# Kernel tuning notes

Measured on AMD Instinct MI355X. Metric: run time of the kernel, lower is better.

The kernel has to match this reference:

```python
import jax, jax.numpy as jnp
import numpy as np
from jax import lax

T, B, D_IN, H = 512, 128, 512, 512


def setup_inputs() -> dict:
    key = jax.random.key(0)
    k1, k2, k3, k4 = jax.random.split(key, 4)
    ins = jax.random.normal(k1, (T, B, D_IN), dtype=jnp.float32)
    resets = jax.random.bernoulli(k2, 0.05, (T, B))  # episode-boundary reset mask
    carry = jnp.zeros((B, H), dtype=jnp.float32)
    # fused GRU weights: gate order (r, z, n); input denses have no bias in flax GRUCell
    Wi = jax.random.normal(k3, (D_IN, 3 * H), dtype=jnp.float32) * (1.0 / np.sqrt(D_IN))
    Wh = jax.random.normal(k4, (H, 3 * H), dtype=jnp.float32) * (1.0 / np.sqrt(H))
    bh = jnp.zeros((3 * H,), dtype=jnp.float32)
    return {"carry": carry, "ins": ins, "resets": resets, "Wi": Wi, "Wh": Wh, "bh": bh}


def reference(carry, ins, resets, Wi, Wh, bh):
    """ScannedRNN forward: scan a flax GRUCell over time with per-step reset masking.

    Returns (final_carry [B,H], ys [T,B,H]).
    """

    def step(h, xr):
        x, r_mask = xr                       # x: [B,D_in], r_mask: [B]
        h = jnp.where(r_mask[:, None], jnp.zeros_like(h), h)
        gi = x @ Wi                          # [B,3H]  (no input bias in flax GRUCell)
        gh = h @ Wh + bh                     # [B,3H]
        ir, iz, inn = jnp.split(gi, 3, axis=-1)
        hr, hz, hn = jnp.split(gh, 3, axis=-1)
        r = jax.nn.sigmoid(ir + hr)
        z = jax.nn.sigmoid(iz + hz)
        n = jnp.tanh(inn + r * hn)
        new_h = (1.0 - z) * n + z * h
        return new_h, new_h                  # GRUCell returns (new_carry, new_carry)

    final_carry, ys = lax.scan(step, carry, (ins, resets))
    return final_carry, ys
```

## Files before the change

### kernel.cpp

```cpp
#include <hip/hip_runtime.h>

#define T_STEPS 512
#define BATCH   128
#define DIN     512
#define HDIM    512
#define THREEH  1536
#define THREADS 256
#define LDK     520
#define LDG     49
#define NGROUP  4
#define NSLICE  32
#define BC      32
#define HC      16
#define NC      48
#define CNT_STRIDE 16
#define SPIN_MAX (1 << 16)
#define EX_DWORDS (NSLICE * BATCH * HC / 2)
#define NG4 8
#define RW4 16
#define NS4 32
#define EXSLOT 131072
#define FLAGS_OFF  0
#define GBAR_OFF   1088
#define DEC_OFF    1280
#define VD_OFF     2048
#define HS_OFF     3072
#define EX_OFF     4096
#define GI_OFF     (1u<<20)
#define GI_BYTES   201326592ULL

typedef _Float16 half8 __attribute__((ext_vector_type(8)));
typedef _Float16 half4v __attribute__((ext_vector_type(4)));
typedef float    f32x4 __attribute__((ext_vector_type(4)));
typedef unsigned int uint4v __attribute__((ext_vector_type(4)));

__global__ void sniff_kernel(const unsigned int* __restrict__ w,
                             unsigned int* __restrict__ dec) {
  unsigned int local = 0;
  for (int i = threadIdx.x; i < (T_STEPS * BATCH) / 4; i += THREADS) {
    if (w[i] > 1u) local = 1u;
  }
  if (local) atomicOr(dec, 1u);
}

__device__ __forceinline__ void run_gemm(const _Float16* __restrict__ sAa,
                                         const _Float16* __restrict__ sW,
                                         float* __restrict__ sAcc,
                                         int wid, int lane) {
  const int fr = lane & 15;
  const int kb = (lane >> 4) * 8;
  for (int tile = wid; tile < 6; tile += 4) {
    int mi = tile / 3, ni = tile - mi * 3;
    const _Float16* ap = sAa + (mi * 16 + fr) * LDK + kb;
    const _Float16* bp = sW  + (ni * 16 + fr) * LDK + kb;
    f32x4 acc = {0.f, 0.f, 0.f, 0.f};
#pragma unroll
    for (int kk = 0; kk < DIN / 32; ++kk)
      acc = __builtin_amdgcn_mfma_f32_16x16x32_f16(
          *(const half8*)(ap + kk * 32),
          *(const half8*)(bp + kk * 32), acc, 0, 0, 0);
    int crow = mi * 16 + (lane >> 4) * 4;
    int ccol = ni * 16 + fr;
#pragma unroll
    for (int j = 0; j < 4; ++j) sAcc[(crow + j) * LDG + ccol] = acc[j];
  }
}

__global__ __launch_bounds__(THREADS, 1)
void gru_kernel_v1(const float* __restrict__ carry,
                   const float* __restrict__ ins,
                   const void*  __restrict__ resets_raw,
                   const float* __restrict__ Wi,
                   const float* __restrict__ Wh,
                   const float* __restrict__ bh,
                   float* __restrict__ out,
                   unsigned int* __restrict__ cnt,
                   unsigned int* __restrict__ ex0,
                   unsigned int* __restrict__ ex1,
                   const unsigned int* __restrict__ dec)
{
  __shared__ alignas(16) _Float16 sWi[NC * LDK];
  __shared__ alignas(16) _Float16 sWh[NC * LDK];
  __shared__ alignas(16) _Float16 sA [BC * LDK];
  __shared__ float sGi[BC * LDG];
  __shared__ float sGh[BC * LDG];
  __shared__ float sBh[NC];
  __shared__ int   sRst[BC];

  const int tid  = threadIdx.x;
  const int bid  = blockIdx.x;
  const int g    = bid & (NGROUP - 1);
  const int p    = bid >> 2;
  const int row0 = g * BC;
  const int col0 = p * HC;

  float* carryOut = out;
  float* ys = out + BATCH * HDIM;

  const unsigned int isBool = *dec;
  const unsigned char* r8  = (const unsigned char*)resets_raw;
  const int*           r32 = (const int*)resets_raw;

  unsigned int* ex[2] = { ex0, ex1 };
  unsigned int* myCnt = cnt + g * CNT_STRIDE;

  for (int idx = tid; idx < DIN * NC; idx += THREADS) {
    int k  = idx / NC;
    int ci = idx - k * NC;
    int gcol = (ci >> 4) * HDIM + col0 + (ci & 15);
    sWi[ci * LDK + k] = (_Float16)Wi[k * THREEH + gcol];
    sWh[ci * LDK + k] = (_Float16)Wh[k * THREEH + gcol];
  }
  if (tid < NC) {
    int gcol = (tid >> 4) * HDIM + col0 + (tid & 15);
    sBh[tid] = bh[gcol];
  }

  float hreg[2];
  {
    int idx = tid * 2;
    int b0 = idx >> 4, c0 = idx & 15;
    hreg[0] = carry[(size_t)(row0 + b0) * HDIM + col0 + c0];
    hreg[1] = carry[(size_t)(row0 + b0) * HDIM + col0 + c0 + 1];
  }

  const int wid  = tid >> 6;
  const int lane = tid & 63;

  auto stageRst = [&](int t) {
    if (tid < BC) {
      int off = t * BATCH + row0 + tid;
      sRst[tid] = isBool ? (int)r8[off] : r32[off];
    }
  };
  auto stageX = [&](int t) {
    const float4* src = (const float4*)(ins + (size_t)(t * BATCH + row0) * DIN);
    for (int i = tid; i < BC * (DIN / 4); i += THREADS) {
      int r = i >> 7, c4 = i & 127;
      float4 v = src[(size_t)r * 128 + c4];
      half4v hv = {(_Float16)v.x, (_Float16)v.y, (_Float16)v.z, (_Float16)v.w};
      *(half4v*)&sA[r * LDK + c4 * 4] = hv;
    }
  };

  stageRst(0);
  stageX(0);
  __syncthreads();
  run_gemm(sA, sWi, sGi, wid, lane);
  __syncthreads();
  {
    const float4* src = (const float4*)(carry + (size_t)row0 * HDIM);
    for (int i = tid; i < BC * (HDIM / 4); i += THREADS) {
      int r = i >> 7, c4 = i & 127;
      float4 v = src[(size_t)r * 128 + c4];
      float m = sRst[r] ? 0.f : 1.f;
      half4v hv = {(_Float16)(v.x*m), (_Float16)(v.y*m),
                   (_Float16)(v.z*m), (_Float16)(v.w*m)};
      *(half4v*)&sA[r * LDK + c4 * 4] = hv;
    }
  }
  __syncthreads();

  for (int t = 0; t < T_STEPS; ++t) {
    if (t > 0) {
      {
        const unsigned int target = 32u * (unsigned)t;
        unsigned int fv;
        for (int it = 0; it < SPIN_MAX; ++it) {
          asm volatile("global_load_dword %0, %1, off sc0 sc1\n\t"
                       "s_waitcnt vmcnt(0)"
                       : "=v"(fv) : "v"(myCnt) : "memory");
          if (fv >= target) break;
          __builtin_amdgcn_s_sleep(1);
        }
      }
      {
        const unsigned int* exsrc = ex[(t - 1) & 1];
        uint4v vv[8];
#pragma unroll
        for (int j = 0; j < 8; ++j) {
          int i = tid + THREADS * j;
          int p_ = i >> 6, b_ = (i >> 1) & 31, hw = (i & 1) << 2;
          const unsigned int* sp = exsrc + p_ * 1024 + (row0 + b_) * 8 + hw;
          asm volatile("global_load_dwordx4 %0, %1, off sc0 sc1"
                       : "=&v"(vv[j]) : "v"(sp) : "memory");
        }
        asm volatile("s_waitcnt vmcnt(0)" ::: "memory");
        __builtin_amdgcn_sched_barrier(0);
#pragma unroll
        for (int j = 0; j < 8; ++j) {
          int i = tid + THREADS * j;
          int p_ = i >> 6, b_ = (i >> 1) & 31, hw = (i & 1) << 3;
          half8 hv = *reinterpret_cast<half8*>(&vv[j]);
          half8 z = {(_Float16)0, (_Float16)0, (_Float16)0, (_Float16)0,
                     (_Float16)0, (_Float16)0, (_Float16)0, (_Float16)0};
          hv = sRst[b_] ? z : hv;
          *(half8*)&sA[b_ * LDK + p_ * 16 + hw] = hv;
        }
      }
      __syncthreads();
    }

    run_gemm(sA, sWh, sGh, wid, lane);
    __syncthreads();

    {
#pragma unroll
      for (int e = 0; e < 2; ++e) {
        int idx = tid * 2 + e;
        int b = idx >> 4, cj = idx & 15;
        float gir = sGi[b * LDG + cj];
        float giz = sGi[b * LDG + 16 + cj];
        float gin = sGi[b * LDG + 32 + cj];
        float ghr = sGh[b * LDG + cj]      + sBh[cj];
        float ghz = sGh[b * LDG + 16 + cj] + sBh[16 + cj];
        float ghn = sGh[b * LDG + 32 + cj] + sBh[32 + cj];
        float r = 1.f / (1.f + __expf(-(gir + ghr)));
        float z = 1.f / (1.f + __expf(-(giz + ghz)));
        float n = tanhf(gin + r * ghn);
        float hp = sRst[b] ? 0.f : hreg[e];
        hreg[e] = (1.f - z) * n + z * hp;
      }
      union { _Float16 h[2]; unsigned int u; } pk;
      pk.h[0] = (_Float16)hreg[0];
      pk.h[1] = (_Float16)hreg[1];
      unsigned int* dst = ex[t & 1] + p * 1024 + (row0 + (tid >> 3)) * 8 + (tid & 7);
      asm volatile("global_store_dword %0, %1, off sc0 sc1"
                   :: "v"(dst), "v"(pk.u) : "memory");
      int b0 = (tid * 2) >> 4, c0 = (tid * 2) & 15;
      float2 yv = make_float2(hreg[0], hreg[1]);
      *(float2*)&ys[((size_t)t * BATCH + row0 + b0) * HDIM + col0 + c0] = yv;
      if (t == T_STEPS - 1)
        *(float2*)&carryOut[(size_t)(row0 + b0) * HDIM + col0 + c0] = yv;
    }
    asm volatile("s_waitcnt vmcnt(0)" ::: "memory");
    __syncthreads();
    if (tid == 0) atomicAdd(myCnt, 1u);

    if (t < T_STEPS - 1) {
      stageRst(t + 1);
      stageX(t + 1);
      __syncthreads();
      run_gemm(sA, sWi, sGi, wid, lane);
      __syncthreads();
    }
  }
}

__global__ __launch_bounds__(256, 1)
void gi_prepass2(const float* __restrict__ ins,
                 const float* __restrict__ Wi,
                 _Float16* __restrict__ gis)
{
  __shared__ alignas(16) _Float16 sWiT[48 * LDK];
  __shared__ alignas(16) _Float16 sX[32 * LDK];

  const int tid = threadIdx.x;
  const int bid = blockIdx.x;
  const int n   = bid >> 3;
  const int mg  = bid & 7;
  const int wid = tid >> 6;
  const int lane = tid & 63;
  const int fr = lane & 15;
  const int kb = (lane >> 4) * 8;

  for (int idx = tid; idx < 48 * DIN; idx += 256) {
    int ci = idx % 48, k = idx / 48;
    int gcol = (ci >> 4) * HDIM + n * 16 + (ci & 15);
    sWiT[ci * LDK + k] = (_Float16)Wi[(size_t)k * THREEH + gcol];
  }

  float4 va[16];
  auto LOADS = [&](int ch) {
    const float4* src = (const float4*)(ins + (size_t)(mg * 8192 + ch * 32) * DIN);
#pragma unroll
    for (int j = 0; j < 16; ++j) va[j] = src[tid + 256 * j];
  };
  auto WRITE = [&]() {
#pragma unroll
    for (int j = 0; j < 16; ++j) {
      int i = tid + 256 * j;
      int r = i >> 7, c4 = i & 127;
      float4 v = va[j];
      half4v hv = {(_Float16)v.x, (_Float16)v.y, (_Float16)v.z, (_Float16)v.w};
      *(half4v*)&sX[r * LDK + c4 * 4] = hv;
    }
  };

  LOADS(0);
  for (int ch = 0; ch < 256; ++ch) {
    WRITE();
    __syncthreads();
    if (ch + 1 < 256) LOADS(ch + 1);

    const int m0 = mg * 8192 + ch * 32;
    const int tt = m0 >> 7;
    const int bb0 = m0 & 127;
    for (int tile = wid; tile < 6; tile += 4) {
      int mi = tile / 3, ni = tile - mi * 3;
      const _Float16* ap = sX   + (mi * 16 + fr) * LDK + kb;
      const _Float16* bp = sWiT + (ni * 16 + fr) * LDK + kb;
      f32x4 acc = {0.f, 0.f, 0.f, 0.f};
#pragma unroll
      for (int kk = 0; kk < DIN / 32; ++kk)
        acc = __builtin_amdgcn_mfma_f32_16x16x32_f16(
            *(const half8*)(ap + kk * 32),
            *(const half8*)(bp + kk * 32), acc, 0, 0, 0);
      int gr = mi * 16 + ((lane >> 4) << 2);
      int col = n * 16 + fr;
      size_t base = ((size_t)(tt * 3 + ni) * BATCH) * HDIM + col;
#pragma unroll
      for (int j = 0; j < 4; ++j)
        gis[base + (size_t)(bb0 + gr + j) * HDIM] = (_Float16)acc[j];
    }
    __syncthreads();
  }
}

__device__ __forceinline__ void gridbar(unsigned int* ctr, int tid) {
  __syncthreads();
  if (tid == 0) {
    atomicAdd(ctr, 1u);
    unsigned int v;
    for (int it = 0; it < SPIN_MAX; ++it) {
      asm volatile("global_load_dword %0, %1, off sc0 sc1\n\t"
                   "s_waitcnt vmcnt(0)" : "=v"(v) : "v"(ctr) : "memory");
      if (v >= 256u) break;
      __builtin_amdgcn_s_sleep(1);
    }
  }
  __syncthreads();
}

__global__ __launch_bounds__(256, 1)
void gru_kernel_v4(const float* __restrict__ carry,
                   const void*  __restrict__ resets_raw,
                   const float* __restrict__ Wh,
                   const float* __restrict__ bh,
                   float* __restrict__ out,
                   unsigned int* __restrict__ wsb,
                   const _Float16* __restrict__ gis,
                   const unsigned int* __restrict__ dec)
{
  __shared__ alignas(16) _Float16 sWh[NC * LDK];
  __shared__ alignas(16) _Float16 sA [RW4 * LDK];
  __shared__ float sGh[RW4 * LDG];
  __shared__ float sBh[NC];
  __shared__ int   sRst[RW4];
  __shared__ int   sFast;

  const int tid  = threadIdx.x;
  const int bid  = blockIdx.x;
  const int g    = bid & 7;
  const int p    = bid >> 3;
  const int row0 = g * RW4;
  const int col0 = p * HC;

  unsigned int* flags = wsb + (FLAGS_OFF / 4) ;
  unsigned int* gbars = wsb + (GBAR_OFF / 4);
  unsigned int* vd    = wsb + (VD_OFF / 4);
  unsigned int* hs    = wsb + (HS_OFF / 4);
  char*         exb   = (char*)wsb + EX_OFF;

  float* carryOut = out;
  float* ys = out + BATCH * HDIM;

  const unsigned int isBool = *dec;
  const unsigned char* r8  = (const unsigned char*)resets_raw;
  const int*           r32 = (const int*)resets_raw;

  bool ok1 = true, ok2 = true;
  {
    unsigned int PAT1 = 0xC0DE0000u | (unsigned)bid;
    unsigned int PAT2 = 0xFACE0000u | (unsigned)bid;
    if (tid == 0) {
      unsigned int* hp = hs + bid;
      asm volatile("global_store_dword %0, %1, off sc0\n\t"
                   "s_waitcnt vmcnt(0)" :: "v"(hp), "v"(PAT1) : "memory");
    }
    gridbar(gbars + 0 * 16, tid);
    if (tid < 32) {
      int peer = g + 8 * tid;
      unsigned int v;
      const unsigned int* hp = hs + peer;
      asm volatile("global_load_dword %0, %1, off sc0\n\t"
                   "s_waitcnt vmcnt(0)" : "=v"(v) : "v"(hp) : "memory");
      ok1 = (v == (0xC0DE0000u | (unsigned)peer));
    }
    gridbar(gbars + 1 * 16, tid);
    if (tid == 0) {
      unsigned int* hp = hs + bid;
      asm volatile("global_store_dword %0, %1, off sc0\n\t"
                   "s_waitcnt vmcnt(0)" :: "v"(hp), "v"(PAT2) : "memory");
    }
    gridbar(gbars + 2 * 16, tid);
    if (tid < 32) {
      int peer = g + 8 * tid;
      unsigned int v;
      const unsigned int* hp = hs + peer;
      asm volatile("global_load_dword %0, %1, off sc0\n\t"
                   "s_waitcnt vmcnt(0)" : "=v"(v) : "v"(hp) : "memory");
      ok2 = (v == (0xFACE0000u | (unsigned)peer));
    }
    bool myok = (tid < 32) ? (ok1 && ok2) : true;
    bool wgok = __all(myok);
    if (tid == 0) {
      unsigned int vv = wgok ? 1u : 0u;
      unsigned int* vp = vd + bid;
      asm volatile("global_store_dword %0, %1, off sc0 sc1\n\t"
                   "s_waitcnt vmcnt(0)" :: "v"(vp), "v"(vv) : "memory");
    }
    gridbar(gbars + 3 * 16, tid);
    bool fin = true;
    if (tid < 32) {
      int peer = g + 8 * tid;
      unsigned int v;
      const unsigned int* vp = vd + peer;
      asm volatile("global_load_dword %0, %1, off sc0 sc1\n\t"
                   "s_waitcnt vmcnt(0)" : "=v"(v) : "v"(vp) : "memory");
      fin = (v == 1u);
    }
    bool unan = __all((tid < 32) ? fin : true);
    if (tid == 0) sFast = unan ? 1 : 0;
    __syncthreads();
  }
  const int fast = sFast;

  if (tid == 0) {
    unsigned int* fp = flags + (g * 32 + p);
    unsigned int zz = 0u;
    if (fast) {
      asm volatile("global_store_dword %0, %1, off sc0\n\t"
                   "s_waitcnt vmcnt(0)" :: "v"(fp), "v"(zz) : "memory");
    } else {
      asm volatile("global_store_dword %0, %1, off sc0 sc1\n\t"
                   "s_waitcnt vmcnt(0)" :: "v"(fp), "v"(zz) : "memory");
    }
  }
  gridbar(gbars + 4 * 16, tid);

  for (int idx = tid; idx < DIN * NC; idx += THREADS) {
    int k  = idx / NC;
    int ci = idx - k * NC;
    int gcol = (ci >> 4) * HDIM + col0 + (ci & 15);
    sWh[ci * LDK + k] = (_Float16)Wh[k * THREEH + gcol];
  }
  if (tid < NC) {
    int gcol = (tid >> 4) * HDIM + col0 + (tid & 15);
    sBh[tid] = bh[gcol];
  }

  const int gb = tid >> 4;
  const int gc = tid & 15;
  float hreg = carry[(size_t)(row0 + gb) * HDIM + col0 + gc];

  const int wid  = tid >> 6;
  const int lane = tid & 63;
  const int fr   = lane & 15;
  const int kb   = (lane >> 4) * 8;

  if (tid < RW4) {
    int off = row0 + tid;
    sRst[tid] = isBool ? (int)r8[off] : r32[off];
  }
  __syncthreads();
  {
    const float4* src = (const float4*)(carry + (size_t)row0 * HDIM);
    for (int i = tid; i < RW4 * (HDIM / 4); i += THREADS) {
      int r = i >> 7, c4 = i & 127;
      float4 v = src[(size_t)r * 128 + c4];
      float m = sRst[r] ? 0.f : 1.f;
      half4v hv = {(_Float16)(v.x*m), (_Float16)(v.y*m),
                   (_Float16)(v.z*m), (_Float16)(v.w*m)};
      *(half4v*)&sA[r * LDK + c4 * 4] = hv;
    }
  }

  const unsigned short* gisu = (const unsigned short*)gis;

  for (int t = 0; t < T_STEPS; ++t) {
    unsigned short gu0, gu1, gu2;
    {
      size_t base = ((size_t)(t * 3) * BATCH + row0 + gb) * HDIM + col0 + gc;
      gu0 = gisu[base];
      gu1 = gisu[base + (size_t)BATCH * HDIM];
      gu2 = gisu[base + 2 * (size_t)BATCH * HDIM];
    }
    if (t > 0 && tid < RW4) {
      int off = t * BATCH + row0 + tid;
      sRst[tid] = isBool ? (int)r8[off] : r32[off];
    }
    if (t > 0) {
      bool done = false;
      const unsigned int* fp = flags + (g * 32 + (tid & 31));
      for (int it = 0; it < SPIN_MAX && !done; ++it) {
        unsigned int fv = 0xFFFFFFFFu;
        if (tid < 32) {
          if (fast) {
            asm volatile("global_load_dword %0, %1, off sc0\n\t"
                         "s_waitcnt vmcnt(0)" : "=v"(fv) : "v"(fp) : "memory");
          } else {
            asm volatile("global_load_dword %0, %1, off sc0 sc1\n\t"
                         "s_waitcnt vmcnt(0)" : "=v"(fv) : "v"(fp) : "memory");
          }
        }
        done = __all((tid < 32) ? (fv >= (unsigned)t) : true);
        if (!done) __builtin_amdgcn_s_sleep(1);
      }
    }
    __syncthreads();

    if (t > 0) {
      const char* src = exb + ((t - 1) & 1) * EXSLOT + g * 16384
                      + (tid >> 4) * 1024 + (tid & 15) * 64;
      uint4v v0, v1, v2, v3;
      if (fast) {
        asm volatile("global_load_dwordx4 %0, %4, off sc0\n\t"
                     "global_load_dwordx4 %1, %4, off offset:16 sc0\n\t"
                     "global_load_dwordx4 %2, %4, off offset:32 sc0\n\t"
                     "global_load_dwordx4 %3, %4, off offset:48 sc0\n\t"
                     "s_waitcnt vmcnt(0)"
                     : "=&v"(v0), "=&v"(v1), "=&v"(v2), "=&v"(v3)
                     : "v"(src) : "memory");
      } else {
        asm volatile("global_load_dwordx4 %0, %4, off sc0 sc1\n\t"
                     "global_load_dwordx4 %1, %4, off offset:16 sc0 sc1\n\t"
                     "global_load_dwordx4 %2, %4, off offset:32 sc0 sc1\n\t"
                     "global_load_dwordx4 %3, %4, off offset:48 sc0 sc1\n\t"
                     "s_waitcnt vmcnt(0)"
                     : "=&v"(v0), "=&v"(v1), "=&v"(v2), "=&v"(v3)
                     : "v"(src) : "memory");
      }
      __builtin_amdgcn_sched_barrier(0);
      int r = tid >> 4, c0 = (tid & 15) * 32;
      half8 h0 = *reinterpret_cast<half8*>(&v0);
      half8 h1 = *reinterpret_cast<half8*>(&v1);
      half8 h2 = *reinterpret_cast<half8*>(&v2);
      half8 h3 = *reinterpret_cast<half8*>(&v3);
      half8 z = {(_Float16)0, (_Float16)0, (_Float16)0, (_Float16)0,
                 (_Float16)0, (_Float16)0, (_Float16)0, (_Float16)0};
      if (sRst[r]) { h0 = z; h1 = z; h2 = z; h3 = z; }
      *(half8*)&sA[r * LDK + c0 +  0] = h0;
      *(half8*)&sA[r * LDK + c0 +  8] = h1;
      *(half8*)&sA[r * LDK + c0 + 16] = h2;
      *(half8*)&sA[r * LDK + c0 + 24] = h3;
      __syncthreads();
    }

    if (wid < 3) {
      const int ni = wid;
      const _Float16* ap = sA  + fr * LDK + kb;
      const _Float16* bp = sWh + (ni * 16 + fr) * LDK + kb;
      f32x4 a0 = {0.f, 0.f, 0.f, 0.f}, a1 = {0.f, 0.f, 0.f, 0.f};
#pragma unroll
      for (int kk = 0; kk < DIN / 32; kk += 2) {
        a0 = __builtin_amdgcn_mfma_f32_16x16x32_f16(
            *(const half8*)(ap + kk * 32), *(const half8*)(bp + kk * 32), a0, 0, 0, 0);
        a1 = __builtin_amdgcn_mfma_f32_16x16x32_f16(
            *(const half8*)(ap + (kk + 1) * 32), *(const half8*)(bp + (kk + 1) * 32), a1, 0, 0, 0);
      }
      a0 += a1;
      int crow = (lane >> 4) * 4;
      int ccol = ni * 16 + fr;
#pragma unroll
      for (int j = 0; j < 4; ++j) sGh[(crow + j) * LDG + ccol] = a0[j];
    }
    __syncthreads();

    {
      union { unsigned short u; _Float16 h; } c0_, c1_, c2_;
      c0_.u = gu0; c1_.u = gu1; c2_.u = gu2;
      float gir = (float)c0_.h;
      float giz = (float)c1_.h;
      float gin = (float)c2_.h;
      float ghr = sGh[gb * LDG + gc]      + sBh[gc];
      float ghz = sGh[gb * LDG + 16 + gc] + sBh[16 + gc];
      float ghn = sGh[gb * LDG + 32 + gc] + sBh[32 + gc];
      float r = 1.f / (1.f + __expf(-(gir + ghr)));
      float z = 1.f / (1.f + __expf(-(giz + ghz)));
      float n = tanhf(gin + r * ghn);
      float hp = sRst[gb] ? 0.f : hreg;
      hreg = (1.f - z) * n + z * hp;

      union { _Float16 h; unsigned short u; } pk;
      pk.h = (_Float16)hreg;
      unsigned int pv = (unsigned int)pk.u;
      unsigned short* dst = (unsigned short*)
        (exb + (t & 1) * EXSLOT + g * 16384 + gb * 1024 + (col0 + gc) * 2);
      if (fast) {
        asm volatile("global_store_short %0, %1, off sc0"
                     :: "v"(dst), "v"(pv) : "memory");
      } else {
        asm volatile("global_store_short %0, %1, off sc0 sc1"
                     :: "v"(dst), "v"(pv) : "memory");
      }
    }
    asm volatile("s_waitcnt vmcnt(0)" ::: "memory");
    __syncthreads();
    if (tid == 0) {
      unsigned int* fp = flags + (g * 32 + p);
      unsigned int val = (unsigned)(t + 1);
      if (fast) {
        asm volatile("global_store_dword %0, %1, off sc0"
                     :: "v"(fp), "v"(val) : "memory");
      } else {
        asm volatile("global_store_dword %0, %1, off sc0 sc1"
                     :: "v"(fp), "v"(val) : "memory");
      }
    }
    {
      ys[((size_t)t * BATCH + row0 + gb) * HDIM + col0 + gc] = hreg;
      if (t == T_STEPS - 1)
        carryOut[(size_t)(row0 + gb) * HDIM + col0 + gc] = hreg;
    }
  }

  __builtin_amdgcn_fence(__ATOMIC_RELEASE, "agent");
}

extern "C" void kernel_launch(void* const* d_in, const int* in_sizes, int n_in,
                              void* d_out, int out_size, void* d_ws, size_t ws_size,
                              hipStream_t stream) {
  const float* carry  = (const float*)d_in[0];
  const float* ins    = (const float*)d_in[1];
  const void*  resets = (const void*)d_in[2];
  const float* Wi     = (const float*)d_in[3];
  const float* Wh     = (const float*)d_in[4];
  const float* bh     = (const float*)d_in[5];
  float* out = (float*)d_out;

  unsigned int* wsb  = (unsigned int*)d_ws;
  unsigned int* dec  = (unsigned int*)((char*)d_ws + DEC_OFF);
  unsigned int* ex0  = (unsigned int*)((char*)d_ws + EX_OFF);
  unsigned int* ex1  = ex0 + EX_DWORDS;
  _Float16*     gis  = (_Float16*)((char*)d_ws + GI_OFF);

  (void)hipMemsetAsync(d_ws, 0, 4096, stream);

  sniff_kernel<<<dim3(1), dim3(THREADS), 0, stream>>>(
      (const unsigned int*)resets, dec);

  const bool bigWs = ws_size >= (size_t)GI_OFF + GI_BYTES;

  if (bigWs) {
    gi_prepass2<<<dim3(256), dim3(256), 0, stream>>>(ins, Wi, gis);
    void* args[] = { (void*)&carry, (void*)&resets, (void*)&Wh, (void*)&bh,
                     (void*)&out, (void*)&wsb, (void*)&gis, (void*)&dec };
    (void)hipLaunchCooperativeKernel((const void*)gru_kernel_v4,
                                     dim3(256), dim3(256),
                                     args, 0, stream);
  } else {
    void* args[] = { (void*)&carry, (void*)&ins, (void*)&resets, (void*)&Wi,
                     (void*)&Wh, (void*)&bh, (void*)&out, (void*)&wsb,
                     (void*)&ex0, (void*)&ex1, (void*)&dec };
    (void)hipLaunchCooperativeKernel((const void*)gru_kernel_v1,
                                     dim3(NGROUP * NSLICE), dim3(THREADS),
                                     args, 0, stream);
  }
}
```

Before: 2.140 ms.

## Load exchanged hidden state straight into MFMA registers and prefetch gate inputs

In the fast path, the MFMA waves now load the peer-exchanged fp16 hidden state directly from global memory into A-fragment registers. This skips the staging pass through shared memory and one block barrier per step. A spare wave prefetches the precomputed input-gate values two steps ahead into a double-buffered shared array, reset flags for all timesteps are preloaded into shared memory, and the spin-wait only sleeps after many polls. The coherence probe now uses a per-launch nonce so stale workspace contents cannot pass as a valid handshake. The fast and slow paths are also split into separate loops, which makes the kernel larger and more complex.

```diff
diff --git a/kernel.cpp b/kernel.cpp
--- a/kernel.cpp
+++ b/kernel.cpp
@@ -16,13 +16,12 @@
 #define CNT_STRIDE 16
 #define SPIN_MAX (1 << 16)
 #define EX_DWORDS (NSLICE * BATCH * HC / 2)
-#define NG4 8
-#define RW4 16
-#define NS4 32
+#define RW5 16
 #define EXSLOT 131072
 #define FLAGS_OFF  0
-#define GBAR_OFF   1088
-#define DEC_OFF    1280
+#define GBAR_OFF   1024
+#define NONCE_OFF  1536
+#define DEC_OFF    1664
 #define VD_OFF     2048
 #define HS_OFF     3072
 #define EX_OFF     4096
@@ -333,7 +332,7 @@
 }
 
 __global__ __launch_bounds__(256, 1)
-void gru_kernel_v4(const float* __restrict__ carry,
+void gru_kernel_v5(const float* __restrict__ carry,
                    const void*  __restrict__ resets_raw,
                    const float* __restrict__ Wh,
                    const float* __restrict__ bh,
@@ -343,24 +342,27 @@
                    const unsigned int* __restrict__ dec)
 {
   __shared__ alignas(16) _Float16 sWh[NC * LDK];
-  __shared__ alignas(16) _Float16 sA [RW4 * LDK];
-  __shared__ float sGh[RW4 * LDG];
+  __shared__ alignas(16) _Float16 sA [RW5 * LDK];
+  __shared__ float sGh[RW5 * LDG];
+  __shared__ alignas(16) _Float16 sGi[2 * 3 * 16 * 16];
   __shared__ float sBh[NC];
-  __shared__ int   sRst[RW4];
+  __shared__ char  sRstAll[T_STEPS * RW5];
   __shared__ int   sFast;
+  __shared__ unsigned int sNonce;
 
   const int tid  = threadIdx.x;
   const int bid  = blockIdx.x;
   const int g    = bid & 7;
   const int p    = bid >> 3;
-  const int row0 = g * RW4;
+  const int row0 = g * RW5;
   const int col0 = p * HC;
 
-  unsigned int* flags = wsb + (FLAGS_OFF / 4) ;
-  unsigned int* gbars = wsb + (GBAR_OFF / 4);
-  unsigned int* vd    = wsb + (VD_OFF / 4);
-  unsigned int* hs    = wsb + (HS_OFF / 4);
-  char*         exb   = (char*)wsb + EX_OFF;
+  unsigned int* flags    = wsb + (FLAGS_OFF / 4);
+  unsigned int* gbars    = wsb + (GBAR_OFF / 4);
+  unsigned int* nonceArr = wsb + (NONCE_OFF / 4);
+  unsigned int* vd       = wsb + (VD_OFF / 4);
+  unsigned int* hs       = wsb + (HS_OFF / 4);
+  char*         exb      = (char*)wsb + EX_OFF;
 
   float* carryOut = out;
   float* ys = out + BATCH * HDIM;
@@ -368,76 +370,14 @@
   const unsigned int isBool = *dec;
   const unsigned char* r8  = (const unsigned char*)resets_raw;
   const int*           r32 = (const int*)resets_raw;
-
-  bool ok1 = true, ok2 = true;
-  {
-    unsigned int PAT1 = 0xC0DE0000u | (unsigned)bid;
-    unsigned int PAT2 = 0xFACE0000u | (unsigned)bid;
-    if (tid == 0) {
-      unsigned int* hp = hs + bid;
-      asm volatile("global_store_dword %0, %1, off sc0\n\t"
-                   "s_waitcnt vmcnt(0)" :: "v"(hp), "v"(PAT1) : "memory");
-    }
-    gridbar(gbars + 0 * 16, tid);
-    if (tid < 32) {
-      int peer = g + 8 * tid;
-      unsigned int v;
-      const unsigned int* hp = hs + peer;
-      asm volatile("global_load_dword %0, %1, off sc0\n\t"
-                   "s_waitcnt vmcnt(0)" : "=v"(v) : "v"(hp) : "memory");
-      ok1 = (v == (0xC0DE0000u | (unsigned)peer));
-    }
-    gridbar(gbars + 1 * 16, tid);
-    if (tid == 0) {
-      unsigned int* hp = hs + bid;
-      asm volatile("global_store_dword %0, %1, off sc0\n\t"
-                   "s_waitcnt vmcnt(0)" :: "v"(hp), "v"(PAT2) : "memory");
-    }
-    gridbar(gbars + 2 * 16, tid);
-    if (tid < 32) {
-      int peer = g + 8 * tid;
-      unsigned int v;
-      const unsigned int* hp = hs + peer;
-      asm volatile("global_load_dword %0, %1, off sc0\n\t"
-                   "s_waitcnt vmcnt(0)" : "=v"(v) : "v"(hp) : "memory");
-      ok2 = (v == (0xFACE0000u | (unsigned)peer));
-    }
-    bool myok = (tid < 32) ? (ok1 && ok2) : true;
-    bool wgok = __all(myok);
-    if (tid == 0) {
-      unsigned int vv = wgok ? 1u : 0u;
-      unsigned int* vp = vd + bid;
-      asm volatile("global_store_dword %0, %1, off sc0 sc1\n\t"
-                   "s_waitcnt vmcnt(0)" :: "v"(vp), "v"(vv) : "memory");
-    }
-    gridbar(gbars + 3 * 16, tid);
-    bool fin = true;
-    if (tid < 32) {
-      int peer = g + 8 * tid;
-      unsigned int v;
-      const unsigned int* vp = vd + peer;
-      asm volatile("global_load_dword %0, %1, off sc0 sc1\n\t"
-                   "s_waitcnt vmcnt(0)" : "=v"(v) : "v"(vp) : "memory");
-      fin = (v == 1u);
-    }
-    bool unan = __all((tid < 32) ? fin : true);
-    if (tid == 0) sFast = unan ? 1 : 0;
-    __syncthreads();
-  }
-  const int fast = sFast;
-
-  if (tid == 0) {
-    unsigned int* fp = flags + (g * 32 + p);
-    unsigned int zz = 0u;
-    if (fast) {
-      asm volatile("global_store_dword %0, %1, off sc0\n\t"
-                   "s_waitcnt vmcnt(0)" :: "v"(fp), "v"(zz) : "memory");
-    } else {
-      asm volatile("global_store_dword %0, %1, off sc0 sc1\n\t"
-                   "s_waitcnt vmcnt(0)" :: "v"(fp), "v"(zz) : "memory");
-    }
-  }
-  gridbar(gbars + 4 * 16, tid);
+  const unsigned short* gisu = (const unsigned short*)gis;
+
+  const int wid  = tid >> 6;
+  const int lane = tid & 63;
+  const int fr   = lane & 15;
+  const int kb   = (lane >> 4) * 8;
+  const int gb   = tid >> 4;
+  const int gc   = tid & 15;
 
   for (int idx = tid; idx < DIN * NC; idx += THREADS) {
     int k  = idx / NC;
@@ -449,80 +389,233 @@
     int gcol = (tid >> 4) * HDIM + col0 + (tid & 15);
     sBh[tid] = bh[gcol];
   }
-
-  const int gb = tid >> 4;
-  const int gc = tid & 15;
+  for (int idx = tid; idx < T_STEPS * RW5; idx += THREADS) {
+    int tt = idx >> 4, r = idx & 15;
+    int off = tt * BATCH + row0 + r;
+    sRstAll[idx] = isBool ? (char)(r8[off] != 0) : (char)(r32[off] != 0);
+  }
   float hreg = carry[(size_t)(row0 + gb) * HDIM + col0 + gc];
 
-  const int wid  = tid >> 6;
-  const int lane = tid & 63;
-  const int fr   = lane & 15;
-  const int kb   = (lane >> 4) * 8;
-
-  if (tid < RW4) {
-    int off = row0 + tid;
-    sRst[tid] = isBool ? (int)r8[off] : r32[off];
+  if (p == 0 && tid == 0) {
+    unsigned long long tv = __builtin_amdgcn_s_memrealtime();
+    unsigned int nv = (unsigned int)(tv ^ (tv >> 32));
+    if (nv == 0) nv = 0x5A5A5A5Au;
+    unsigned int* np = nonceArr + g;
+    asm volatile("global_store_dword %0, %1, off sc0 sc1\n\t"
+                 "s_waitcnt vmcnt(0)" :: "v"(np), "v"(nv) : "memory");
+  }
+  gridbar(gbars + 0 * 16, tid);
+  if (tid == 0) {
+    unsigned int nv;
+    asm volatile("global_load_dword %0, %1, off sc0 sc1\n\t"
+                 "s_waitcnt vmcnt(0)" : "=v"(nv) : "v"(nonceArr + g) : "memory");
+    sNonce = nv;
   }
   __syncthreads();
+  const unsigned int nonce = sNonce;
+
+  bool okAll = true;
+  for (int r = 0; r < 2; ++r) {
+    gridbar(gbars + (1 + r) * 16, tid);
+    if (tid == 0) {
+      unsigned int tok = nonce ^ ((unsigned)p << 8) ^ ((unsigned)(r + 1) << 20);
+      asm volatile("global_store_dword %0, %1, off sc0\n\t"
+                   "s_waitcnt vmcnt(0)" :: "v"(hs + bid), "v"(tok) : "memory");
+    }
+    __syncthreads();
+    for (int s = 0; s < 40; ++s) __builtin_amdgcn_s_sleep(2);
+    if (tid < 32) {
+      unsigned int v;
+      const unsigned int* hp = hs + (g + 8 * tid);
+      asm volatile("global_load_dword %0, %1, off sc0\n\t"
+                   "s_waitcnt vmcnt(0)" : "=v"(v) : "v"(hp) : "memory");
+      unsigned int expv = nonce ^ ((unsigned)tid << 8) ^ ((unsigned)(r + 1) << 20);
+      okAll = okAll && (v == expv);
+    }
+  }
   {
-    const float4* src = (const float4*)(carry + (size_t)row0 * HDIM);
-    for (int i = tid; i < RW4 * (HDIM / 4); i += THREADS) {
-      int r = i >> 7, c4 = i & 127;
-      float4 v = src[(size_t)r * 128 + c4];
-      float m = sRst[r] ? 0.f : 1.f;
-      half4v hv = {(_Float16)(v.x*m), (_Float16)(v.y*m),
-                   (_Float16)(v.z*m), (_Float16)(v.w*m)};
-      *(half4v*)&sA[r * LDK + c4 * 4] = hv;
-    }
-  }
-
-  const unsigned short* gisu = (const unsigned short*)gis;
+    bool wgok = __all((tid < 32) ? okAll : true);
+    if (tid == 0) {
+      unsigned int vv = wgok ? 1u : 0u;
+      asm volatile("global_store_dword %0, %1, off sc0 sc1\n\t"
+                   "s_waitcnt vmcnt(0)" :: "v"(vd + bid), "v"(vv) : "memory");
+    }
+    gridbar(gbars + 3 * 16, tid);
+    bool fin = true;
+    if (tid < 32) {
+      unsigned int v;
+      asm volatile("global_load_dword %0, %1, off sc0 sc1\n\t"
+                   "s_waitcnt vmcnt(0)" : "=v"(v) : "v"(vd + (g + 8 * tid)) : "memory");
+      fin = (v == 1u);
+    }
+    bool unan = __all((tid < 32) ? fin : true);
+    if (tid == 0) sFast = unan ? 1 : 0;
+    __syncthreads();
+  }
+  const int fast = sFast;
+
+  if (tid == 0) {
+    unsigned int* fp = flags + (g * 32 + p);
+    unsigned int zz = 0u;
+    if (fast) asm volatile("global_store_dword %0, %1, off sc0\n\ts_waitcnt vmcnt(0)" :: "v"(fp), "v"(zz) : "memory");
+    else      asm volatile("global_store_dword %0, %1, off sc0 sc1\n\ts_waitcnt vmcnt(0)" :: "v"(fp), "v"(zz) : "memory");
+  }
+  {
+    union { _Float16 h; unsigned short u; } ck;
+    ck.h = (_Float16)hreg;
+    unsigned int cv = (unsigned int)ck.u;
+    char* cdst = exb + EXSLOT + g * 16384 + gb * 1024 + (col0 + gc) * 2;
+    if (fast) asm volatile("global_store_short %0, %1, off sc0" :: "v"(cdst), "v"(cv) : "memory");
+    else      asm volatile("global_store_short %0, %1, off sc0 sc1" :: "v"(cdst), "v"(cv) : "memory");
+    asm volatile("s_waitcnt vmcnt(0)" ::: "memory");
+  }
+  gridbar(gbars + 4 * 16, tid);
+
+  {
+    size_t base = ((size_t)0 * BATCH + row0 + gb) * HDIM + col0 + gc;
+    unsigned short v0 = gisu[base];
+    unsigned short v1 = gisu[base + (size_t)BATCH * HDIM];
+    unsigned short v2 = gisu[base + 2 * (size_t)BATCH * HDIM];
+    union { unsigned short u; _Float16 h; } c;
+    c.u = v0; sGi[(0 * 16 + gb) * 16 + gc] = c.h;
+    c.u = v1; sGi[(1 * 16 + gb) * 16 + gc] = c.h;
+    c.u = v2; sGi[(2 * 16 + gb) * 16 + gc] = c.h;
+  }
+  uint4v w3a = {0, 0, 0, 0}, w3b = {0, 0, 0, 0};
+  if (fast && wid == 3 && lane < 48) {
+    int gamma = lane >> 4, row = lane & 15;
+    const char* sp = (const char*)(gisu + ((size_t)(1 * 3 + gamma) * BATCH + row0 + row) * HDIM + col0);
+    asm volatile("global_load_dwordx4 %0, %2, off\n\t"
+                 "global_load_dwordx4 %1, %2, off offset:16"
+                 : "=v"(w3a), "=v"(w3b) : "v"(sp) : "memory");
+  }
+  __syncthreads();
 
   for (int t = 0; t < T_STEPS; ++t) {
-    unsigned short gu0, gu1, gu2;
-    {
-      size_t base = ((size_t)(t * 3) * BATCH + row0 + gb) * HDIM + col0 + gc;
-      gu0 = gisu[base];
-      gu1 = gisu[base + (size_t)BATCH * HDIM];
-      gu2 = gisu[base + 2 * (size_t)BATCH * HDIM];
-    }
-    if (t > 0 && tid < RW4) {
-      int off = t * BATCH + row0 + tid;
-      sRst[tid] = isBool ? (int)r8[off] : r32[off];
-    }
-    if (t > 0) {
-      bool done = false;
-      const unsigned int* fp = flags + (g * 32 + (tid & 31));
-      for (int it = 0; it < SPIN_MAX && !done; ++it) {
+    const int slot = t & 1;
+    if (fast) {
+      if (t > 0) {
         unsigned int fv = 0xFFFFFFFFu;
-        if (tid < 32) {
-          if (fast) {
+        const unsigned int* fp = flags + g * 32 + (tid & 31);
+        bool done = false;
+        for (int it = 0; it < SPIN_MAX && !done; ++it) {
+          if (tid < 32)
             asm volatile("global_load_dword %0, %1, off sc0\n\t"
                          "s_waitcnt vmcnt(0)" : "=v"(fv) : "v"(fp) : "memory");
-          } else {
+          done = __all((tid < 32) ? (fv >= (unsigned)t) : true);
+          if (!done && it > 256) __builtin_amdgcn_s_sleep(1);
+        }
+      }
+      __syncthreads();
+
+      if (wid < 3) {
+        const char* abase = exb + (slot ^ 1) * EXSLOT + g * 16384 + fr * 1024 + kb * 2;
+        uint4v af[16];
+#pragma unroll
+        for (int kk = 0; kk < 16; ++kk) {
+          const char* sp = abase + kk * 64;
+          asm volatile("global_load_dwordx4 %0, %1, off sc0"
+                       : "=v"(af[kk]) : "v"(sp) : "memory");
+        }
+        asm volatile("s_waitcnt vmcnt(0)" ::: "memory");
+        __builtin_amdgcn_sched_barrier(0);
+        int rr = (int)sRstAll[t * 16 + fr];
+        if (rr) {
+#pragma unroll
+          for (int kk = 0; kk < 16; ++kk) af[kk] = (uint4v){0, 0, 0, 0};
+        }
+        const _Float16* bp = sWh + (wid * 16 + fr) * LDK + kb;
+        f32x4 a0 = {0.f, 0.f, 0.f, 0.f}, a1 = {0.f, 0.f, 0.f, 0.f};
+#pragma unroll
+        for (int kk = 0; kk < 16; kk += 2) {
+          a0 = __builtin_amdgcn_mfma_f32_16x16x32_f16(
+              *(half8*)&af[kk], *(const half8*)(bp + kk * 32), a0, 0, 0, 0);
+          a1 = __builtin_amdgcn_mfma_f32_16x16x32_f16(
+              *(half8*)&af[kk + 1], *(const half8*)(bp + (kk + 1) * 32), a1, 0, 0, 0);
+        }
+        a0 += a1;
+        int crow = (lane >> 4) * 4;
+        int ccol = wid * 16 + fr;
+#pragma unroll
+        for (int j = 0; j < 4; ++j) sGh[(crow + j) * LDG + ccol] = a0[j];
+      } else {
+        asm volatile("s_waitcnt vmcnt(0)" ::: "memory");
+        __builtin_amdgcn_sched_barrier(0);
+        if (lane < 48) {
+          int gamma = lane >> 4, row = lane & 15;
+          _Float16* d = &sGi[((t + 1) & 1) * 768 + (gamma * 16 + row) * 16];
+          *(uint4v*)d = w3a;
+          *(uint4v*)(d + 8) = w3b;
+        }
+        int tn = (t + 2 < T_STEPS) ? t + 2 : T_STEPS - 1;
+        if (lane < 48) {
+          int gamma = lane >> 4, row = lane & 15;
+          const char* sp = (const char*)(gisu + ((size_t)(tn * 3 + gamma) * BATCH + row0 + row) * HDIM + col0);
+          asm volatile("global_load_dwordx4 %0, %2, off\n\t"
+                       "global_load_dwordx4 %1, %2, off offset:16"
+                       : "=v"(w3a), "=v"(w3b) : "v"(sp) : "memory");
+        }
+      }
+      __syncthreads();
+
+      {
+        float gir = (float)sGi[slot * 768 + (0 * 16 + gb) * 16 + gc];
+        float giz = (float)sGi[slot * 768 + (1 * 16 + gb) * 16 + gc];
+        float gin = (float)sGi[slot * 768 + (2 * 16 + gb) * 16 + gc];
+        float ghr = sGh[gb * LDG + gc]      + sBh[gc];
+        float ghz = sGh[gb * LDG + 16 + gc] + sBh[16 + gc];
+        float ghn = sGh[gb * LDG + 32 + gc] + sBh[32 + gc];
+        float r = 1.f / (1.f + __expf(-(gir + ghr)));
+        float z = 1.f / (1.f + __expf(-(giz + ghz)));
+        float n = tanhf(gin + r * ghn);
+        float hp = sRstAll[t * 16 + gb] ? 0.f : hreg;
+        hreg = (1.f - z) * n + z * hp;
+        if (t < T_STEPS - 1) {
+          union { _Float16 h; unsigned short u; } pk;
+          pk.h = (_Float16)hreg;
+          unsigned int pv = (unsigned int)pk.u;
+          char* dst = exb + slot * EXSLOT + g * 16384 + gb * 1024 + (col0 + gc) * 2;
+          asm volatile("global_store_short %0, %1, off sc0"
+                       :: "v"(dst), "v"(pv) : "memory");
+        }
+      }
+      asm volatile("s_waitcnt vmcnt(0)" ::: "memory");
+      __syncthreads();
+      if (tid == 0 && t < T_STEPS - 1) {
+        unsigned int* fp = flags + (g * 32 + p);
+        unsigned int val = (unsigned)(t + 1);
+        asm volatile("global_store_dword %0, %1, off sc0"
+                     :: "v"(fp), "v"(val) : "memory");
+      }
+      ys[((size_t)t * BATCH + row0 + gb) * HDIM + col0 + gc] = hreg;
+      if (t == T_STEPS - 1)
+        carryOut[(size_t)(row0 + gb) * HDIM + col0 + gc] = hreg;
+    } else {
+      unsigned short fg0, fg1, fg2;
+      {
+        size_t base = ((size_t)(t * 3) * BATCH + row0 + gb) * HDIM + col0 + gc;
+        fg0 = gisu[base];
+        fg1 = gisu[base + (size_t)BATCH * HDIM];
+        fg2 = gisu[base + 2 * (size_t)BATCH * HDIM];
+      }
+      if (t > 0) {
+        unsigned int fv = 0xFFFFFFFFu;
+        const unsigned int* fp = flags + g * 32 + (tid & 31);
+        bool done = false;
+        for (int it = 0; it < SPIN_MAX && !done; ++it) {
+          if (tid < 32)
             asm volatile("global_load_dword %0, %1, off sc0 sc1\n\t"
                          "s_waitcnt vmcnt(0)" : "=v"(fv) : "v"(fp) : "memory");
-          }
-        }
-        done = __all((tid < 32) ? (fv >= (unsigned)t) : true);
-        if (!done) __builtin_amdgcn_s_sleep(1);
-      }
-    }
-    __syncthreads();
-
-    if (t > 0) {
-      const char* src = exb + ((t - 1) & 1) * EXSLOT + g * 16384
-                      + (tid >> 4) * 1024 + (tid & 15) * 64;
-      uint4v v0, v1, v2, v3;
-      if (fast) {
-        asm volatile("global_load_dwordx4 %0, %4, off sc0\n\t"
-                     "global_load_dwordx4 %1, %4, off offset:16 sc0\n\t"
-                     "global_load_dwordx4 %2, %4, off offset:32 sc0\n\t"
-                     "global_load_dwordx4 %3, %4, off offset:48 sc0\n\t"
-                     "s_waitcnt vmcnt(0)"
-                     : "=&v"(v0), "=&v"(v1), "=&v"(v2), "=&v"(v3)
-                     : "v"(src) : "memory");
-      } else {
+          done = __all((tid < 32) ? (fv >= (unsigned)t) : true);
+          if (!done) __builtin_amdgcn_s_sleep(1);
+        }
+      }
+      __syncthreads();
+
+      {
+        const char* src = exb + (slot ^ 1) * EXSLOT + g * 16384
+                        + (tid >> 4) * 1024 + (tid & 15) * 64;
+        uint4v v0, v1, v2, v3;
         asm volatile("global_load_dwordx4 %0, %4, off sc0 sc1\n\t"
                      "global_load_dwordx4 %1, %4, off offset:16 sc0 sc1\n\t"
                      "global_load_dwordx4 %2, %4, off offset:32 sc0 sc1\n\t"
@@ -530,85 +623,72 @@
                      "s_waitcnt vmcnt(0)"
                      : "=&v"(v0), "=&v"(v1), "=&v"(v2), "=&v"(v3)
                      : "v"(src) : "memory");
-      }
-      __builtin_amdgcn_sched_barrier(0);
-      int r = tid >> 4, c0 = (tid & 15) * 32;
-      half8 h0 = *reinterpret_cast<half8*>(&v0);
-      half8 h1 = *reinterpret_cast<half8*>(&v1);
-      half8 h2 = *reinterpret_cast<half8*>(&v2);
-      half8 h3 = *reinterpret_cast<half8*>(&v3);
-      half8 z = {(_Float16)0, (_Float16)0, (_Float16)0, (_Float16)0,
-                 (_Float16)0, (_Float16)0, (_Float16)0, (_Float16)0};
-      if (sRst[r]) { h0 = z; h1 = z; h2 = z; h3 = z; }
-      *(half8*)&sA[r * LDK + c0 +  0] = h0;
-      *(half8*)&sA[r * LDK + c0 +  8] = h1;
-      *(half8*)&sA[r * LDK + c0 + 16] = h2;
-      *(half8*)&sA[r * LDK + c0 + 24] = h3;
-      __syncthreads();
-    }
-
-    if (wid < 3) {
-      const int ni = wid;
-      const _Float16* ap = sA  + fr * LDK + kb;
-      const _Float16* bp = sWh + (ni * 16 + fr) * LDK + kb;
-      f32x4 a0 = {0.f, 0.f, 0.f, 0.f}, a1 = {0.f, 0.f, 0.f, 0.f};
-#pragma unroll
-      for (int kk = 0; kk < DIN / 32; kk += 2) {
-        a0 = __builtin_amdgcn_mfma_f32_16x16x32_f16(
-            *(const half8*)(ap + kk * 32), *(const half8*)(bp + kk * 32), a0, 0, 0, 0);
-        a1 = __builtin_amdgcn_mfma_f32_16x16x32_f16(
-            *(const half8*)(ap + (kk + 1) * 32), *(const half8*)(bp + (kk + 1) * 32), a1, 0, 0, 0);
-      }
-      a0 += a1;
-      int crow = (lane >> 4) * 4;
-      int ccol = ni * 16 + fr;
-#pragma unroll
-      for (int j = 0; j < 4; ++j) sGh[(crow + j) * LDG + ccol] = a0[j];
-    }
-    __syncthreads();
-
-    {
-      union { unsigned short u; _Float16 h; } c0_, c1_, c2_;
-      c0_.u = gu0; c1_.u = gu1; c2_.u = gu2;
-      float gir = (float)c0_.h;
-      float giz = (float)c1_.h;
-      float gin = (float)c2_.h;
-      float ghr = sGh[gb * LDG + gc]      + sBh[gc];
-      float ghz = sGh[gb * LDG + 16 + gc] + sBh[16 + gc];
-      float ghn = sGh[gb * LDG + 32 + gc] + sBh[32 + gc];
-      float r = 1.f / (1.f + __expf(-(gir + ghr)));
-      float z = 1.f / (1.f + __expf(-(giz + ghz)));
-      float n = tanhf(gin + r * ghn);
-      float hp = sRst[gb] ? 0.f : hreg;
-      hreg = (1.f - z) * n + z * hp;
-
-      union { _Float16 h; unsigned short u; } pk;
-      pk.h = (_Float16)hreg;
-      unsigned int pv = (unsigned int)pk.u;
-      unsigned short* dst = (unsigned short*)
-        (exb + (t & 1) * EXSLOT + g * 16384 + gb * 1024 + (col0 + gc) * 2);
-      if (fast) {
-        asm volatile("global_store_short %0, %1, off sc0"
-                     :: "v"(dst), "v"(pv) : "memory");
-      } else {
-        asm volatile("global_store_short %0, %1, off sc0 sc1"
-                     :: "v"(dst), "v"(pv) : "memory");
-      }
-    }
-    asm volatile("s_waitcnt vmcnt(0)" ::: "memory");
-    __syncthreads();
-    if (tid == 0) {
-      unsigned int* fp = flags + (g * 32 + p);
-      unsigned int val = (unsigned)(t + 1);
-      if (fast) {
-        asm volatile("global_store_dword %0, %1, off sc0"
-                     :: "v"(fp), "v"(val) : "memory");
-      } else {
+        __builtin_amdgcn_sched_barrier(0);
+        int r = tid >> 4, c0 = (tid & 15) * 32;
+        half8 h0 = *reinterpret_cast<half8*>(&v0);
+        half8 h1 = *reinterpret_cast<half8*>(&v1);
+        half8 h2 = *reinterpret_cast<half8*>(&v2);
+        half8 h3 = *reinterpret_cast<half8*>(&v3);
+        half8 z = {(_Float16)0, (_Float16)0, (_Float16)0, (_Float16)0,
+                   (_Float16)0, (_Float16)0, (_Float16)0, (_Float16)0};
+        if (sRstAll[t * 16 + r]) { h0 = z; h1 = z; h2 = z; h3 = z; }
+        *(half8*)&sA[r * LDK + c0 +  0] = h0;
+        *(half8*)&sA[r * LDK + c0 +  8] = h1;
+        *(half8*)&sA[r * LDK + c0 + 16] = h2;
+        *(half8*)&sA[r * LDK + c0 + 24] = h3;
+      }
+      __syncthreads();
+
+      if (wid < 3) {
+        const _Float16* ap = sA  + fr * LDK + kb;
+        const _Float16* bp = sWh + (wid * 16 + fr) * LDK + kb;
+        f32x4 a0 = {0.f, 0.f, 0.f, 0.f}, a1 = {0.f, 0.f, 0.f, 0.f};
+#pragma unroll
+        for (int kk = 0; kk < 16; kk += 2) {
+          a0 = __builtin_amdgcn_mfma_f32_16x16x32_f16(
+              *(const half8*)(ap + kk * 32), *(const half8*)(bp + kk * 32), a0, 0, 0, 0);
+          a1 = __builtin_amdgcn_mfma_f32_16x16x32_f16(
+              *(const half8*)(ap + (kk + 1) * 32), *(const half8*)(bp + (kk + 1) * 32), a1, 0, 0, 0);
+        }
+        a0 += a1;
+        int crow = (lane >> 4) * 4;
+        int ccol = wid * 16 + fr;
+#pragma unroll
+        for (int j = 0; j < 4; ++j) sGh[(crow + j) * LDG + ccol] = a0[j];
+      }
+      __syncthreads();
+
+      {
+        union { unsigned short u; _Float16 h; } c0_, c1_, c2_;
+        c0_.u = fg0; c1_.u = fg1; c2_.u = fg2;
+        float gir = (float)c0_.h;
+        float giz = (float)c1_.h;
+        float gin = (float)c2_.h;
+        float ghr = sGh[gb * LDG + gc]      + sBh[gc];
+        float ghz = sGh[gb * LDG + 16 + gc] + sBh[16 + gc];
+        float ghn = sGh[gb * LDG + 32 + gc] + sBh[32 + gc];
+        float r = 1.f / (1.f + __expf(-(gir + ghr)));
+        float z = 1.f / (1.f + __expf(-(giz + ghz)));
+        float n = tanhf(gin + r * ghn);
+        float hp = sRstAll[t * 16 + gb] ? 0.f : hreg;
+        hreg = (1.f - z) * n + z * hp;
+        if (t < T_STEPS - 1) {
+          union { _Float16 h; unsigned short u; } pk;
+          pk.h = (_Float16)hreg;
+          unsigned int pv = (unsigned int)pk.u;
+          char* dst = exb + slot * EXSLOT + g * 16384 + gb * 1024 + (col0 + gc) * 2;
+          asm volatile("global_store_short %0, %1, off sc0 sc1"
+                       :: "v"(dst), "v"(pv) : "memory");
+        }
+      }
+      asm volatile("s_waitcnt vmcnt(0)" ::: "memory");
+      __syncthreads();
+      if (tid == 0 && t < T_STEPS - 1) {
+        unsigned int* fp = flags + (g * 32 + p);
+        unsigned int val = (unsigned)(t + 1);
         asm volatile("global_store_dword %0, %1, off sc0 sc1"
                      :: "v"(fp), "v"(val) : "memory");
       }
-    }
-    {
       ys[((size_t)t * BATCH + row0 + gb) * HDIM + col0 + gc] = hreg;
       if (t == T_STEPS - 1)
         carryOut[(size_t)(row0 + gb) * HDIM + col0 + gc] = hreg;
@@ -646,7 +726,7 @@
     gi_prepass2<<<dim3(256), dim3(256), 0, stream>>>(ins, Wi, gis);
     void* args[] = { (void*)&carry, (void*)&resets, (void*)&Wh, (void*)&bh,
                      (void*)&out, (void*)&wsb, (void*)&gis, (void*)&dec };
-    (void)hipLaunchCooperativeKernel((const void*)gru_kernel_v4,
+    (void)hipLaunchCooperativeKernel((const void*)gru_kernel_v5,
                                      dim3(256), dim3(256),
                                      args, 0, stream);
   } else {
```

New measurement: 2.273 ms. +6.2%, slower.
